# Kernel optimization log

Measured on AMD Instinct MI355X. Metric: run time of the kernel, lower is better.

Reference implementation:

```python
import jax, jax.numpy as jnp
import numpy as np

EMB = 128  # embsize
WORD = 128  # word_size
ITERS = 2


def _agg(embeds, neibors):
    # embeds: [B, N, D], neibors: [B, N, K] indices into node axis N (per batch)
    # mean-pool gathered neighbor embeddings -> [B, N, D]
    gathered = jax.vmap(lambda e, idx: e[idx])(embeds, neibors)  # [B, N, K, D]
    return gathered.mean(axis=2)


def setup_inputs() -> dict:
    key = jax.random.key(0)
    ks = jax.random.split(key, 9)
    B, N, K = 64, 512, 16
    word_embs = jax.random.normal(ks[0], (B, N, WORD), dtype=jnp.float32)
    lib_embs = jax.random.normal(ks[1], (B, N, WORD), dtype=jnp.float32)
    neibors = jax.random.randint(ks[2], (B, N, K), 0, N)
    neibors_lib = jax.random.randint(ks[3], (B, N, K), 0, N)
    mask = jax.random.uniform(ks[4], (B, N), dtype=jnp.float32)
    # xavier-uniform style params
    def xav(k, shape):
        bound = float(np.sqrt(6.0 / (shape[0] + shape[1])))
        return jax.random.uniform(k, shape, dtype=jnp.float32, minval=-bound, maxval=bound)
    weight = xav(ks[5], (WORD, EMB))
    weight2 = xav(ks[6], (EMB, EMB))
    enc_w1 = xav(ks[7], (WORD, EMB))
    enc_w2 = xav(ks[8], (EMB, EMB))
    return {"word_embs": word_embs, "neibors": neibors, "lib_embs": lib_embs,
            "neibors_lib": neibors_lib, "mask": mask, "weight": weight,
            "weight2": weight2, "enc_w1": enc_w1, "enc_w2": enc_w2}


def reference(word_embs, neibors, lib_embs, neibors_lib, mask, weight, weight2, enc_w1, enc_w2):
    B, N, _ = word_embs.shape
    # lib aggregation is loop-invariant (lib_embs fixed); same math as in-loop recompute
    agg_lib = jnp.einsum('bnw,we->bne', _agg(lib_embs, neibors_lib), weight)  # [B, N, EMB]
    word_proj = jnp.einsum('bnw,we->bne', word_embs, enc_w1)  # loop-invariant
    last_embed = jnp.zeros((B, N, EMB), dtype=jnp.float32)
    for _ in range(ITERS):
        agg_func = _agg(last_embed, neibors)  # [B, N, EMB]
        last_embed = jnp.tanh(word_proj + jnp.einsum('bne,ef->bnf', agg_func, enc_w2) + agg_lib)
    # masked sum over nodes, then final linear
    pooled = (last_embed * mask[:, :, None]).sum(axis=1)  # [B, EMB]
    return pooled @ weight2
```

## Files before the change

### kernel.cpp

```cpp
#include <hip/hip_runtime.h>
#include <hip/hip_bf16.h>

#define B_   64
#define N_   512
#define K_   16
#define D_   128
#define NPB  16
#define G1   ((B_*N_)/NPB)

typedef float f32x4  __attribute__((ext_vector_type(4)));
typedef short bf16x8 __attribute__((ext_vector_type(8)));

static __device__ __forceinline__ short f2bf(float x) {
    union { float f; unsigned u; } v; v.f = x;
    unsigned r = v.u + 0x7fffu + ((v.u >> 16) & 1u);
    return (short)(r >> 16);
}
static __device__ __forceinline__ float bfbits2f(unsigned hi_bits) {
    return __uint_as_float(hi_bits);
}
static __device__ __forceinline__ float fast_tanh(float x) {
    float e = __expf(2.f * x);
    return 1.f - 2.f * __builtin_amdgcn_rcpf(e + 1.f);
}

__global__ __launch_bounds__(256) void pack_kernel(const float* __restrict__ enc1,
                                                   const float* __restrict__ wgt,
                                                   const float* __restrict__ enc2,
                                                   short* __restrict__ Bp1,
                                                   short* __restrict__ Bp2,
                                                   float* __restrict__ out) {
    int tid = blockIdx.x * 256 + threadIdx.x;
    if (tid < 8192) out[tid] = 0.f;
    short o8[8];
    if (tid < 4096) {
        int l = tid & 63, nt = (tid >> 6) & 7, ks = tid >> 9;
        int k0 = ks * 32 + (l >> 4) * 8;
        int col = nt * 16 + (l & 15);
#pragma unroll
        for (int j = 0; j < 8; ++j) {
            int r = k0 + j;
            float v = (r < 128) ? enc1[r * 128 + col] : wgt[(r - 128) * 128 + col];
            o8[j] = f2bf(v);
        }
        *(int4*)&Bp1[(size_t)tid * 8] = *(int4*)o8;
    } else if (tid < 6144) {
        int t2 = tid - 4096;
        int l = t2 & 63, nt = (t2 >> 6) & 7, ks = t2 >> 9;
        int k0 = ks * 32 + (l >> 4) * 8;
        int col = nt * 16 + (l & 15);
#pragma unroll
        for (int j = 0; j < 8; ++j) o8[j] = f2bf(enc2[(k0 + j) * 128 + col]);
        *(int4*)&Bp2[(size_t)t2 * 8] = *(int4*)o8;
    }
}

static __device__ __forceinline__ int swz_blk() {
    const int hw = blockIdx.x;
    return ((hw & 7) << 8) + (hw >> 3);
}

#define LDA1 264
__global__ __launch_bounds__(256) void gemm1(const float* __restrict__ word,
                                             const int* __restrict__ nbrL,
                                             const float* __restrict__ lib,
                                             const short* __restrict__ Bp1,
                                             float* __restrict__ base,
                                             short* __restrict__ t1) {
    __shared__ short sA[NPB * LDA1];
    __shared__ int sIdx[NPB * 16];
    const int tid = threadIdx.x;
    const int blk = swz_blk();
    const int b = blk >> 5;
    const int node0 = blk * NPB;

    if (tid < 64) *(int4*)&sIdx[tid * 4] = *(const int4*)&nbrL[(size_t)node0 * 16 + tid * 4];
    __syncthreads();

    const int w = tid >> 6, l = tid & 63;
    const int rh = l >> 5, c4 = l & 31;
    const float* libB = lib + (size_t)b * N_ * D_;

#pragma unroll
    for (int p = 0; p < 2; ++p) {
        const int row = 4 * w + 2 * p + rh;
        const int gid = node0 + row;
        float4 wv = *(const float4*)&word[(size_t)gid * D_ + c4 * 4];
        short4 ws; ws.x = f2bf(wv.x); ws.y = f2bf(wv.y); ws.z = f2bf(wv.z); ws.w = f2bf(wv.w);
        *(short4*)&sA[row * LDA1 + c4 * 4] = ws;
        int idxr[16];
#pragma unroll
        for (int k = 0; k < 16; ++k) idxr[k] = sIdx[row * 16 + k];
        float4 s = {0.f, 0.f, 0.f, 0.f};
#pragma unroll
        for (int k = 0; k < 16; ++k) {
            float4 lv = *(const float4*)&libB[(size_t)idxr[k] * D_ + c4 * 4];
            s.x += lv.x; s.y += lv.y; s.z += lv.z; s.w += lv.w;
        }
        short4 as; as.x = f2bf(s.x * 0.0625f); as.y = f2bf(s.y * 0.0625f);
        as.z = f2bf(s.z * 0.0625f); as.w = f2bf(s.w * 0.0625f);
        *(short4*)&sA[row * LDA1 + 128 + c4 * 4] = as;
    }
    __syncthreads();

    f32x4 acc[2];
    acc[0] = (f32x4)0.f; acc[1] = (f32x4)0.f;

    const int arow = l & 15;
#pragma unroll
    for (int ks = 0; ks < 8; ++ks) {
        bf16x8 a = *(const bf16x8*)&sA[arow * LDA1 + ks * 32 + (l >> 4) * 8];
#pragma unroll
        for (int j = 0; j < 2; ++j) {
            const int nt = 2 * w + j;
            bf16x8 bb = *(const bf16x8*)&Bp1[((size_t)(ks * 8 + nt) * 64 + l) * 8];
            acc[j] = __builtin_amdgcn_mfma_f32_16x16x32_bf16(a, bb, acc[j], 0, 0, 0);
        }
    }

    const int r0 = (l >> 4) * 4;
    const int cl = l & 15;
#pragma unroll
    for (int j = 0; j < 2; ++j) {
        const int col = (2 * w + j) * 16 + cl;
#pragma unroll
        for (int r = 0; r < 4; ++r) {
            size_t o = (size_t)(node0 + r0 + r) * D_ + col;
            float v = acc[j][r];
            base[o] = v;
            t1[o] = f2bf(fast_tanh(v));
        }
    }
}

#define LDA2 136
__global__ __launch_bounds__(256) void gemm2(const short* __restrict__ t1,
                                             const int* __restrict__ nbr,
                                             const short* __restrict__ Bp2,
                                             const float* __restrict__ base,
                                             const float* __restrict__ mask,
                                             const float* __restrict__ w2,
                                             float* __restrict__ out) {
    __shared__ short sA[NPB * LDA2];
    __shared__ int sIdx[NPB * 16];
    __shared__ float pred[128];
    const int tid = threadIdx.x;
    const int blk = swz_blk();
    const int b = blk >> 5;
    const int node0 = blk * NPB;

    if (tid < 64) *(int4*)&sIdx[tid * 4] = *(const int4*)&nbr[(size_t)node0 * 16 + tid * 4];
    __syncthreads();

    const int w = tid >> 6, l = tid & 63;
    const int rh = l >> 5, c4 = l & 31;
    const short* t1B = t1 + (size_t)b * N_ * D_;

#pragma unroll
    for (int p = 0; p < 2; ++p) {
        const int row = 4 * w + 2 * p + rh;
        int idxr[16];
#pragma unroll
        for (int k = 0; k < 16; ++k) idxr[k] = sIdx[row * 16 + k];
        float s0 = 0.f, s1 = 0.f, s2 = 0.f, s3 = 0.f;
#pragma unroll
        for (int k = 0; k < 16; ++k) {
            uint2 u = *(const uint2*)&t1B[(size_t)idxr[k] * D_ + c4 * 4];
            s0 += bfbits2f(u.x << 16); s1 += bfbits2f(u.x & 0xffff0000u);
            s2 += bfbits2f(u.y << 16); s3 += bfbits2f(u.y & 0xffff0000u);
        }
        short4 as; as.x = f2bf(s0 * 0.0625f); as.y = f2bf(s1 * 0.0625f);
        as.z = f2bf(s2 * 0.0625f); as.w = f2bf(s3 * 0.0625f);
        *(short4*)&sA[row * LDA2 + c4 * 4] = as;
    }
    __syncthreads();

    f32x4 acc[2];
    acc[0] = (f32x4)0.f; acc[1] = (f32x4)0.f;

    const int arow = l & 15;
#pragma unroll
    for (int ks = 0; ks < 4; ++ks) {
        bf16x8 a = *(const bf16x8*)&sA[arow * LDA2 + ks * 32 + (l >> 4) * 8];
#pragma unroll
        for (int j = 0; j < 2; ++j) {
            const int nt = 2 * w + j;
            bf16x8 bb = *(const bf16x8*)&Bp2[((size_t)(ks * 8 + nt) * 64 + l) * 8];
            acc[j] = __builtin_amdgcn_mfma_f32_16x16x32_bf16(a, bb, acc[j], 0, 0, 0);
        }
    }

    const int r0 = (l >> 4) * 4;
    const int cl = l & 15;
#pragma unroll
    for (int j = 0; j < 2; ++j) {
        const int col = (2 * w + j) * 16 + cl;
        float s = 0.f;
#pragma unroll
        for (int r = 0; r < 4; ++r) {
            size_t o = (size_t)(node0 + r0 + r) * D_ + col;
            float v = fast_tanh(base[o] + acc[j][r]);
            s += v * mask[node0 + r0 + r];
        }
        s += __shfl_xor(s, 16);
        s += __shfl_xor(s, 32);
        if (l < 16) pred[col] = s;
    }
    __syncthreads();
    if (tid < 128) {
        float a2 = 0.f;
#pragma unroll 4
        for (int f = 0; f < 128; ++f) a2 += pred[f] * w2[f * 128 + tid];
        atomicAdd(&out[b * 128 + tid], a2);
    }
}

extern "C" void kernel_launch(void* const* d_in, const int* in_sizes, int n_in,
                              void* d_out, int out_size, void* d_ws, size_t ws_size,
                              hipStream_t stream) {
    const float* word_embs   = (const float*)d_in[0];
    const int*   neibors     = (const int*)d_in[1];
    const float* lib_embs    = (const float*)d_in[2];
    const int*   neibors_lib = (const int*)d_in[3];
    const float* mask        = (const float*)d_in[4];
    const float* weight      = (const float*)d_in[5];
    const float* weight2     = (const float*)d_in[6];
    const float* enc_w1      = (const float*)d_in[7];
    const float* enc_w2      = (const float*)d_in[8];
    float* out = (float*)d_out;

    char* ws = (char*)d_ws;
    float* base = (float*)(ws);
    short* t1   = (short*)(ws + (1u << 24));
    short* Bp1  = (short*)(ws + (1u << 24) + (1u << 23));
    short* Bp2  = (short*)(ws + (1u << 24) + (1u << 23) + 65536);

    pack_kernel<<<32, 256, 0, stream>>>(enc_w1, weight, enc_w2, Bp1, Bp2, out);
    gemm1<<<G1, 256, 0, stream>>>(word_embs, neibors_lib, lib_embs, Bp1, base, t1);
    gemm2<<<G1, 256, 0, stream>>>(t1, neibors, Bp2, base, mask, weight2, out);
}
```

Measured before the change: 51.28 us.

## Pre-convert lib embeddings to bf16 and store base intermediate in bf16

Adds a conversion pass in the prep kernel that turns lib_embs into a bf16 copy, so gemm1's neighbor gather reads half the bytes per neighbor. The base pre-activation written by gemm1 and reread by gemm2 is stored as bf16 instead of fp32, halving that round trip. The mask values are staged in shared memory. It adds an extra full pass over lib_embs and reduces the precision of the intermediate sums.

```diff
diff --git a/kernel.cpp b/kernel.cpp
--- a/kernel.cpp
+++ b/kernel.cpp
@@ -19,19 +19,38 @@
 static __device__ __forceinline__ float bfbits2f(unsigned hi_bits) {
     return __uint_as_float(hi_bits);
 }
+static __device__ __forceinline__ float bf2f(short h) {
+    return __uint_as_float(((unsigned)(unsigned short)h) << 16);
+}
 static __device__ __forceinline__ float fast_tanh(float x) {
     float e = __expf(2.f * x);
     return 1.f - 2.f * __builtin_amdgcn_rcpf(e + 1.f);
 }
 
-__global__ __launch_bounds__(256) void pack_kernel(const float* __restrict__ enc1,
-                                                   const float* __restrict__ wgt,
-                                                   const float* __restrict__ enc2,
-                                                   short* __restrict__ Bp1,
-                                                   short* __restrict__ Bp2,
-                                                   float* __restrict__ out) {
-    int tid = blockIdx.x * 256 + threadIdx.x;
-    if (tid < 8192) out[tid] = 0.f;
+__global__ __launch_bounds__(256) void prep(const float* __restrict__ lib,
+                                            const float* __restrict__ enc1,
+                                            const float* __restrict__ wgt,
+                                            const float* __restrict__ enc2,
+                                            short* __restrict__ libh,
+                                            short* __restrict__ Bp1,
+                                            short* __restrict__ Bp2,
+                                            float* __restrict__ out) {
+    const int blk = blockIdx.x;
+    if (blk < 1024) {
+        const size_t g = ((size_t)blk * 256 + threadIdx.x) * 16;
+        short o16[16];
+#pragma unroll
+        for (int q = 0; q < 4; ++q) {
+            float4 v = *(const float4*)&lib[g + q * 4];
+            o16[q * 4 + 0] = f2bf(v.x); o16[q * 4 + 1] = f2bf(v.y);
+            o16[q * 4 + 2] = f2bf(v.z); o16[q * 4 + 3] = f2bf(v.w);
+        }
+        *(int4*)&libh[g]     = *(int4*)o16;
+        *(int4*)&libh[g + 8] = *(int4*)(o16 + 8);
+        return;
+    }
+    int tid = (blk - 1024) * 256 + threadIdx.x;
+    out[tid] = 0.f;
     short o8[8];
     if (tid < 4096) {
         int l = tid & 63, nt = (tid >> 6) & 7, ks = tid >> 9;
@@ -63,9 +82,9 @@
 #define LDA1 264
 __global__ __launch_bounds__(256) void gemm1(const float* __restrict__ word,
                                              const int* __restrict__ nbrL,
-                                             const float* __restrict__ lib,
+                                             const short* __restrict__ libh,
                                              const short* __restrict__ Bp1,
-                                             float* __restrict__ base,
+                                             short* __restrict__ baseh,
                                              short* __restrict__ t1) {
     __shared__ short sA[NPB * LDA1];
     __shared__ int sIdx[NPB * 16];
@@ -79,7 +98,7 @@
 
     const int w = tid >> 6, l = tid & 63;
     const int rh = l >> 5, c4 = l & 31;
-    const float* libB = lib + (size_t)b * N_ * D_;
+    const short* libB = libh + (size_t)b * N_ * D_;
 
 #pragma unroll
     for (int p = 0; p < 2; ++p) {
@@ -91,14 +110,15 @@
         int idxr[16];
 #pragma unroll
         for (int k = 0; k < 16; ++k) idxr[k] = sIdx[row * 16 + k];
-        float4 s = {0.f, 0.f, 0.f, 0.f};
+        float s0 = 0.f, s1 = 0.f, s2 = 0.f, s3 = 0.f;
 #pragma unroll
         for (int k = 0; k < 16; ++k) {
-            float4 lv = *(const float4*)&libB[(size_t)idxr[k] * D_ + c4 * 4];
-            s.x += lv.x; s.y += lv.y; s.z += lv.z; s.w += lv.w;
-        }
-        short4 as; as.x = f2bf(s.x * 0.0625f); as.y = f2bf(s.y * 0.0625f);
-        as.z = f2bf(s.z * 0.0625f); as.w = f2bf(s.w * 0.0625f);
+            uint2 u = *(const uint2*)&libB[(size_t)idxr[k] * D_ + c4 * 4];
+            s0 += bfbits2f(u.x << 16); s1 += bfbits2f(u.x & 0xffff0000u);
+            s2 += bfbits2f(u.y << 16); s3 += bfbits2f(u.y & 0xffff0000u);
+        }
+        short4 as; as.x = f2bf(s0 * 0.0625f); as.y = f2bf(s1 * 0.0625f);
+        as.z = f2bf(s2 * 0.0625f); as.w = f2bf(s3 * 0.0625f);
         *(short4*)&sA[row * LDA1 + 128 + c4 * 4] = as;
     }
     __syncthreads();
@@ -127,8 +147,8 @@
         for (int r = 0; r < 4; ++r) {
             size_t o = (size_t)(node0 + r0 + r) * D_ + col;
             float v = acc[j][r];
-            base[o] = v;
-            t1[o] = f2bf(fast_tanh(v));
+            baseh[o] = f2bf(v);
+            t1[o]    = f2bf(fast_tanh(v));
         }
     }
 }
@@ -137,19 +157,21 @@
 __global__ __launch_bounds__(256) void gemm2(const short* __restrict__ t1,
                                              const int* __restrict__ nbr,
                                              const short* __restrict__ Bp2,
-                                             const float* __restrict__ base,
+                                             const short* __restrict__ baseh,
                                              const float* __restrict__ mask,
                                              const float* __restrict__ w2,
                                              float* __restrict__ out) {
     __shared__ short sA[NPB * LDA2];
     __shared__ int sIdx[NPB * 16];
     __shared__ float pred[128];
+    __shared__ float smask[NPB];
     const int tid = threadIdx.x;
     const int blk = swz_blk();
     const int b = blk >> 5;
     const int node0 = blk * NPB;
 
     if (tid < 64) *(int4*)&sIdx[tid * 4] = *(const int4*)&nbr[(size_t)node0 * 16 + tid * 4];
+    if (tid >= 64 && tid < 64 + NPB) smask[tid - 64] = mask[node0 + tid - 64];
     __syncthreads();
 
     const int w = tid >> 6, l = tid & 63;
@@ -199,8 +221,8 @@
 #pragma unroll
         for (int r = 0; r < 4; ++r) {
             size_t o = (size_t)(node0 + r0 + r) * D_ + col;
-            float v = fast_tanh(base[o] + acc[j][r]);
-            s += v * mask[node0 + r0 + r];
+            float v = fast_tanh(bf2f(baseh[o]) + acc[j][r]);
+            s += v * smask[r0 + r];
         }
         s += __shfl_xor(s, 16);
         s += __shfl_xor(s, 32);
@@ -230,12 +252,13 @@
     float* out = (float*)d_out;
 
     char* ws = (char*)d_ws;
-    float* base = (float*)(ws);
-    short* t1   = (short*)(ws + (1u << 24));
-    short* Bp1  = (short*)(ws + (1u << 24) + (1u << 23));
-    short* Bp2  = (short*)(ws + (1u << 24) + (1u << 23) + 65536);
-
-    pack_kernel<<<32, 256, 0, stream>>>(enc_w1, weight, enc_w2, Bp1, Bp2, out);
-    gemm1<<<G1, 256, 0, stream>>>(word_embs, neibors_lib, lib_embs, Bp1, base, t1);
-    gemm2<<<G1, 256, 0, stream>>>(t1, neibors, Bp2, base, mask, weight2, out);
-}
+    short* baseh = (short*)(ws);
+    short* t1    = (short*)(ws + (1u << 23));
+    short* libh  = (short*)(ws + (2u << 23));
+    short* Bp1   = (short*)(ws + (3u << 23));
+    short* Bp2   = (short*)(ws + (3u << 23) + 65536);
+
+    prep<<<1056, 256, 0, stream>>>(lib_embs, enc_w1, weight, enc_w2, libh, Bp1, Bp2, out);
+    gemm1<<<G1, 256, 0, stream>>>(word_embs, neibors_lib, libh, Bp1, baseh, t1);
+    gemm2<<<G1, 256, 0, stream>>>(t1, neibors, Bp2, baseh, mask, weight2, out);
+}
```

Result: faster. 49.59 us (-3.3%).

## Project before gathering so neighbor means run on projected bf16 rows

Applied to the files above, without the earlier changes.

Uses linearity of the mean to apply the weight projection before aggregation. A new proj kernel computes bf16 word_proj and lib_proj, k1 gathers the projected lib rows and multiplies tanh(base) by enc_w2, and k2 gathers those products and applies tanh, the mask and the final linear. This halves gather bytes (bf16 instead of fp32 lib rows) and removes the GEMM from the last stage. The cost is an extra kernel launch, an extra full pass writing and reading the projections, and more bf16 rounding in the base and product buffers.

```diff
diff --git a/kernel.cpp b/kernel.cpp
--- a/kernel.cpp
+++ b/kernel.cpp
@@ -5,8 +5,6 @@
 #define N_   512
 #define K_   16
 #define D_   128
-#define NPB  16
-#define G1   ((B_*N_)/NPB)
 
 typedef float f32x4  __attribute__((ext_vector_type(4)));
 typedef short bf16x8 __attribute__((ext_vector_type(8)));
@@ -19,39 +17,87 @@
 static __device__ __forceinline__ float bfbits2f(unsigned hi_bits) {
     return __uint_as_float(hi_bits);
 }
+static __device__ __forceinline__ float bf2f(short h) {
+    return __uint_as_float(((unsigned)(unsigned short)h) << 16);
+}
 static __device__ __forceinline__ float fast_tanh(float x) {
     float e = __expf(2.f * x);
     return 1.f - 2.f * __builtin_amdgcn_rcpf(e + 1.f);
 }
 
-__global__ __launch_bounds__(256) void pack_kernel(const float* __restrict__ enc1,
-                                                   const float* __restrict__ wgt,
-                                                   const float* __restrict__ enc2,
-                                                   short* __restrict__ Bp1,
-                                                   short* __restrict__ Bp2,
-                                                   float* __restrict__ out) {
-    int tid = blockIdx.x * 256 + threadIdx.x;
-    if (tid < 8192) out[tid] = 0.f;
+#define LDX 136
+
+__global__ __launch_bounds__(256) void pack(const float* __restrict__ enc1,
+                                            const float* __restrict__ wgt,
+                                            const float* __restrict__ enc2,
+                                            short* __restrict__ Bp1e,
+                                            short* __restrict__ Bpw,
+                                            short* __restrict__ Bp2,
+                                            float* __restrict__ out) {
+    const int blk = blockIdx.x, t = threadIdx.x;
+    if (blk >= 24) { out[(blk - 24) * 256 + t] = 0.f; return; }
+    const int ptid = blk * 256 + t;
+    const int m3 = ptid >> 11;
+    const int r = ptid & 2047;
+    const int ks = r >> 9, nt = (r >> 6) & 7, l = r & 63;
+    const int k0 = ks * 32 + (l >> 4) * 8;
+    const int col = nt * 16 + (l & 15);
+    const float* src = (m3 == 0) ? enc1 : (m3 == 1) ? wgt : enc2;
+    short* dst = (m3 == 0) ? Bp1e : (m3 == 1) ? Bpw : Bp2;
     short o8[8];
-    if (tid < 4096) {
-        int l = tid & 63, nt = (tid >> 6) & 7, ks = tid >> 9;
-        int k0 = ks * 32 + (l >> 4) * 8;
-        int col = nt * 16 + (l & 15);
-#pragma unroll
-        for (int j = 0; j < 8; ++j) {
-            int r = k0 + j;
-            float v = (r < 128) ? enc1[r * 128 + col] : wgt[(r - 128) * 128 + col];
-            o8[j] = f2bf(v);
-        }
-        *(int4*)&Bp1[(size_t)tid * 8] = *(int4*)o8;
-    } else if (tid < 6144) {
-        int t2 = tid - 4096;
-        int l = t2 & 63, nt = (t2 >> 6) & 7, ks = t2 >> 9;
-        int k0 = ks * 32 + (l >> 4) * 8;
-        int col = nt * 16 + (l & 15);
-#pragma unroll
-        for (int j = 0; j < 8; ++j) o8[j] = f2bf(enc2[(k0 + j) * 128 + col]);
-        *(int4*)&Bp2[(size_t)t2 * 8] = *(int4*)o8;
+#pragma unroll
+    for (int j = 0; j < 8; ++j) o8[j] = f2bf(src[(k0 + j) * 128 + col]);
+    *(int4*)&dst[(size_t)r * 8] = *(int4*)o8;
+}
+
+__global__ __launch_bounds__(256) void proj(const float* __restrict__ word,
+                                            const float* __restrict__ lib,
+                                            const short* __restrict__ Bp1e,
+                                            const short* __restrict__ Bpw,
+                                            short* __restrict__ wordp,
+                                            short* __restrict__ libp) {
+    __shared__ short sX[16 * LDX];
+    const int hw = blockIdx.x, t = threadIdx.x;
+    const int g = hw & 7, q = hw >> 3;
+    const int m = q >> 8;
+    const int Lb = g * 256 + (q & 255);
+    const float* X = m ? lib : word;
+    const short* Bp = m ? Bpw : Bp1e;
+    short* Y = m ? libp : wordp;
+    const size_t rb = (size_t)Lb * 16;
+
+#pragma unroll
+    for (int i = 0; i < 2; ++i) {
+        const int gidx = i * 1024 + t * 4;
+        const int row = gidx >> 7, col = gidx & 127;
+        float4 v = *(const float4*)&X[rb * 128 + gidx];
+        short4 s; s.x = f2bf(v.x); s.y = f2bf(v.y); s.z = f2bf(v.z); s.w = f2bf(v.w);
+        *(short4*)&sX[row * LDX + col] = s;
+    }
+    __syncthreads();
+
+    const int w = t >> 6, l = t & 63;
+    f32x4 acc[2];
+    acc[0] = (f32x4)0.f; acc[1] = (f32x4)0.f;
+    const int arow = l & 15;
+#pragma unroll
+    for (int ks = 0; ks < 4; ++ks) {
+        bf16x8 a = *(const bf16x8*)&sX[arow * LDX + ks * 32 + (l >> 4) * 8];
+#pragma unroll
+        for (int j = 0; j < 2; ++j) {
+            const int nt = 2 * w + j;
+            bf16x8 bb = *(const bf16x8*)&Bp[((size_t)(ks * 8 + nt) * 64 + l) * 8];
+            acc[j] = __builtin_amdgcn_mfma_f32_16x16x32_bf16(a, bb, acc[j], 0, 0, 0);
+        }
+    }
+
+    const int r0 = (l >> 4) * 4, cl = l & 15;
+#pragma unroll
+    for (int j = 0; j < 2; ++j) {
+        const int col = (2 * w + j) * 16 + cl;
+#pragma unroll
+        for (int r = 0; r < 4; ++r)
+            Y[(rb + r0 + r) * 128 + col] = f2bf(acc[j][r]);
     }
 }
 
@@ -60,102 +106,100 @@
     return ((hw & 7) << 8) + (hw >> 3);
 }
 
-#define LDA1 264
-__global__ __launch_bounds__(256) void gemm1(const float* __restrict__ word,
-                                             const int* __restrict__ nbrL,
-                                             const float* __restrict__ lib,
-                                             const short* __restrict__ Bp1,
-                                             float* __restrict__ base,
-                                             short* __restrict__ t1) {
-    __shared__ short sA[NPB * LDA1];
-    __shared__ int sIdx[NPB * 16];
+__global__ __launch_bounds__(256) void k1(const int* __restrict__ nbrL,
+                                          const short* __restrict__ libp,
+                                          const short* __restrict__ wordp,
+                                          const short* __restrict__ Bp2,
+                                          short* __restrict__ baseh,
+                                          short* __restrict__ u) {
+    __shared__ short sA[16 * LDX];
+    __shared__ int sIdx[16 * 16];
     const int tid = threadIdx.x;
     const int blk = swz_blk();
     const int b = blk >> 5;
-    const int node0 = blk * NPB;
+    const int node0 = blk * 16;
 
     if (tid < 64) *(int4*)&sIdx[tid * 4] = *(const int4*)&nbrL[(size_t)node0 * 16 + tid * 4];
     __syncthreads();
 
     const int w = tid >> 6, l = tid & 63;
     const int rh = l >> 5, c4 = l & 31;
-    const float* libB = lib + (size_t)b * N_ * D_;
+    const short* libB = libp + (size_t)b * N_ * D_;
 
 #pragma unroll
     for (int p = 0; p < 2; ++p) {
         const int row = 4 * w + 2 * p + rh;
-        const int gid = node0 + row;
-        float4 wv = *(const float4*)&word[(size_t)gid * D_ + c4 * 4];
-        short4 ws; ws.x = f2bf(wv.x); ws.y = f2bf(wv.y); ws.z = f2bf(wv.z); ws.w = f2bf(wv.w);
-        *(short4*)&sA[row * LDA1 + c4 * 4] = ws;
         int idxr[16];
 #pragma unroll
         for (int k = 0; k < 16; ++k) idxr[k] = sIdx[row * 16 + k];
-        float4 s = {0.f, 0.f, 0.f, 0.f};
+        float s0 = 0.f, s1 = 0.f, s2 = 0.f, s3 = 0.f;
 #pragma unroll
         for (int k = 0; k < 16; ++k) {
-            float4 lv = *(const float4*)&libB[(size_t)idxr[k] * D_ + c4 * 4];
-            s.x += lv.x; s.y += lv.y; s.z += lv.z; s.w += lv.w;
-        }
-        short4 as; as.x = f2bf(s.x * 0.0625f); as.y = f2bf(s.y * 0.0625f);
-        as.z = f2bf(s.z * 0.0625f); as.w = f2bf(s.w * 0.0625f);
-        *(short4*)&sA[row * LDA1 + 128 + c4 * 4] = as;
+            uint2 uu = *(const uint2*)&libB[(size_t)idxr[k] * D_ + c4 * 4];
+            s0 += bfbits2f(uu.x << 16); s1 += bfbits2f(uu.x & 0xffff0000u);
+            s2 += bfbits2f(uu.y << 16); s3 += bfbits2f(uu.y & 0xffff0000u);
+        }
+        short4 wp = *(const short4*)&wordp[(size_t)(node0 + row) * D_ + c4 * 4];
+        float b0 = bf2f(wp.x) + s0 * 0.0625f;
+        float b1 = bf2f(wp.y) + s1 * 0.0625f;
+        float b2 = bf2f(wp.z) + s2 * 0.0625f;
+        float b3 = bf2f(wp.w) + s3 * 0.0625f;
+        short4 bs; bs.x = f2bf(b0); bs.y = f2bf(b1); bs.z = f2bf(b2); bs.w = f2bf(b3);
+        *(short4*)&baseh[(size_t)(node0 + row) * D_ + c4 * 4] = bs;
+        short4 ts; ts.x = f2bf(fast_tanh(b0)); ts.y = f2bf(fast_tanh(b1));
+        ts.z = f2bf(fast_tanh(b2)); ts.w = f2bf(fast_tanh(b3));
+        *(short4*)&sA[row * LDX + c4 * 4] = ts;
     }
     __syncthreads();
 
     f32x4 acc[2];
     acc[0] = (f32x4)0.f; acc[1] = (f32x4)0.f;
-
     const int arow = l & 15;
 #pragma unroll
-    for (int ks = 0; ks < 8; ++ks) {
-        bf16x8 a = *(const bf16x8*)&sA[arow * LDA1 + ks * 32 + (l >> 4) * 8];
+    for (int ks = 0; ks < 4; ++ks) {
+        bf16x8 a = *(const bf16x8*)&sA[arow * LDX + ks * 32 + (l >> 4) * 8];
 #pragma unroll
         for (int j = 0; j < 2; ++j) {
             const int nt = 2 * w + j;
-            bf16x8 bb = *(const bf16x8*)&Bp1[((size_t)(ks * 8 + nt) * 64 + l) * 8];
+            bf16x8 bb = *(const bf16x8*)&Bp2[((size_t)(ks * 8 + nt) * 64 + l) * 8];
             acc[j] = __builtin_amdgcn_mfma_f32_16x16x32_bf16(a, bb, acc[j], 0, 0, 0);
         }
     }
 
-    const int r0 = (l >> 4) * 4;
-    const int cl = l & 15;
+    const int r0 = (l >> 4) * 4, cl = l & 15;
 #pragma unroll
     for (int j = 0; j < 2; ++j) {
         const int col = (2 * w + j) * 16 + cl;
 #pragma unroll
-        for (int r = 0; r < 4; ++r) {
-            size_t o = (size_t)(node0 + r0 + r) * D_ + col;
-            float v = acc[j][r];
-            base[o] = v;
-            t1[o] = f2bf(fast_tanh(v));
-        }
-    }
-}
-
-#define LDA2 136
-__global__ __launch_bounds__(256) void gemm2(const short* __restrict__ t1,
-                                             const int* __restrict__ nbr,
-                                             const short* __restrict__ Bp2,
-                                             const float* __restrict__ base,
-                                             const float* __restrict__ mask,
-                                             const float* __restrict__ w2,
-                                             float* __restrict__ out) {
-    __shared__ short sA[NPB * LDA2];
-    __shared__ int sIdx[NPB * 16];
+        for (int r = 0; r < 4; ++r)
+            u[(size_t)(node0 + r0 + r) * D_ + col] = f2bf(acc[j][r]);
+    }
+}
+
+__global__ __launch_bounds__(256) void k2(const int* __restrict__ nbr,
+                                          const short* __restrict__ u,
+                                          const short* __restrict__ baseh,
+                                          const float* __restrict__ mask,
+                                          const float* __restrict__ w2,
+                                          float* __restrict__ out) {
+    __shared__ int sIdx[16 * 16];
+    __shared__ float smask[16];
+    __shared__ float predp[8][128];
     __shared__ float pred[128];
     const int tid = threadIdx.x;
     const int blk = swz_blk();
     const int b = blk >> 5;
-    const int node0 = blk * NPB;
+    const int node0 = blk * 16;
 
     if (tid < 64) *(int4*)&sIdx[tid * 4] = *(const int4*)&nbr[(size_t)node0 * 16 + tid * 4];
+    if (tid >= 64 && tid < 80) smask[tid - 64] = mask[node0 + tid - 64];
     __syncthreads();
 
     const int w = tid >> 6, l = tid & 63;
     const int rh = l >> 5, c4 = l & 31;
-    const short* t1B = t1 + (size_t)b * N_ * D_;
-
+    const short* uB = u + (size_t)b * N_ * D_;
+
+    float a0 = 0.f, a1 = 0.f, a2c = 0.f, a3 = 0.f;
 #pragma unroll
     for (int p = 0; p < 2; ++p) {
         const int row = 4 * w + 2 * p + rh;
@@ -165,53 +209,36 @@
         float s0 = 0.f, s1 = 0.f, s2 = 0.f, s3 = 0.f;
 #pragma unroll
         for (int k = 0; k < 16; ++k) {
-            uint2 u = *(const uint2*)&t1B[(size_t)idxr[k] * D_ + c4 * 4];
-            s0 += bfbits2f(u.x << 16); s1 += bfbits2f(u.x & 0xffff0000u);
-            s2 += bfbits2f(u.y << 16); s3 += bfbits2f(u.y & 0xffff0000u);
-        }
-        short4 as; as.x = f2bf(s0 * 0.0625f); as.y = f2bf(s1 * 0.0625f);
-        as.z = f2bf(s2 * 0.0625f); as.w = f2bf(s3 * 0.0625f);
-        *(short4*)&sA[row * LDA2 + c4 * 4] = as;
-    }
-    __syncthreads();
-
-    f32x4 acc[2];
-    acc[0] = (f32x4)0.f; acc[1] = (f32x4)0.f;
-
-    const int arow = l & 15;
-#pragma unroll
-    for (int ks = 0; ks < 4; ++ks) {
-        bf16x8 a = *(const bf16x8*)&sA[arow * LDA2 + ks * 32 + (l >> 4) * 8];
-#pragma unroll
-        for (int j = 0; j < 2; ++j) {
-            const int nt = 2 * w + j;
-            bf16x8 bb = *(const bf16x8*)&Bp2[((size_t)(ks * 8 + nt) * 64 + l) * 8];
-            acc[j] = __builtin_amdgcn_mfma_f32_16x16x32_bf16(a, bb, acc[j], 0, 0, 0);
-        }
-    }
-
-    const int r0 = (l >> 4) * 4;
-    const int cl = l & 15;
-#pragma unroll
-    for (int j = 0; j < 2; ++j) {
-        const int col = (2 * w + j) * 16 + cl;
-        float s = 0.f;
-#pragma unroll
-        for (int r = 0; r < 4; ++r) {
-            size_t o = (size_t)(node0 + r0 + r) * D_ + col;
-            float v = fast_tanh(base[o] + acc[j][r]);
-            s += v * mask[node0 + r0 + r];
-        }
-        s += __shfl_xor(s, 16);
-        s += __shfl_xor(s, 32);
-        if (l < 16) pred[col] = s;
-    }
-    __syncthreads();
+            uint2 uu = *(const uint2*)&uB[(size_t)idxr[k] * D_ + c4 * 4];
+            s0 += bfbits2f(uu.x << 16); s1 += bfbits2f(uu.x & 0xffff0000u);
+            s2 += bfbits2f(uu.y << 16); s3 += bfbits2f(uu.y & 0xffff0000u);
+        }
+        short4 bs = *(const short4*)&baseh[(size_t)(node0 + row) * D_ + c4 * 4];
+        const float mk = smask[row];
+        a0 += mk * fast_tanh(bf2f(bs.x) + s0 * 0.0625f);
+        a1 += mk * fast_tanh(bf2f(bs.y) + s1 * 0.0625f);
+        a2c += mk * fast_tanh(bf2f(bs.z) + s2 * 0.0625f);
+        a3 += mk * fast_tanh(bf2f(bs.w) + s3 * 0.0625f);
+    }
+    const int pg = w * 2 + rh;
+    predp[pg][c4 * 4 + 0] = a0;
+    predp[pg][c4 * 4 + 1] = a1;
+    predp[pg][c4 * 4 + 2] = a2c;
+    predp[pg][c4 * 4 + 3] = a3;
+    __syncthreads();
+
     if (tid < 128) {
-        float a2 = 0.f;
+        float tot = 0.f;
+#pragma unroll
+        for (int pgi = 0; pgi < 8; ++pgi) tot += predp[pgi][tid];
+        pred[tid] = tot;
+    }
+    __syncthreads();
+    if (tid < 128) {
+        float acc = 0.f;
 #pragma unroll 4
-        for (int f = 0; f < 128; ++f) a2 += pred[f] * w2[f * 128 + tid];
-        atomicAdd(&out[b * 128 + tid], a2);
+        for (int f = 0; f < 128; ++f) acc += pred[f] * w2[f * 128 + tid];
+        atomicAdd(&out[b * 128 + tid], acc);
     }
 }
 
@@ -230,12 +257,16 @@
     float* out = (float*)d_out;
 
     char* ws = (char*)d_ws;
-    float* base = (float*)(ws);
-    short* t1   = (short*)(ws + (1u << 24));
-    short* Bp1  = (short*)(ws + (1u << 24) + (1u << 23));
-    short* Bp2  = (short*)(ws + (1u << 24) + (1u << 23) + 65536);
-
-    pack_kernel<<<32, 256, 0, stream>>>(enc_w1, weight, enc_w2, Bp1, Bp2, out);
-    gemm1<<<G1, 256, 0, stream>>>(word_embs, neibors_lib, lib_embs, Bp1, base, t1);
-    gemm2<<<G1, 256, 0, stream>>>(t1, neibors, Bp2, base, mask, weight2, out);
-}
+    short* wordp = (short*)(ws);
+    short* libp  = (short*)(ws + (1u << 23));
+    short* ubuf  = (short*)(ws + (2u << 23));
+    short* baseh = (short*)(ws + (3u << 23));
+    short* Bp1e  = (short*)(ws + (4u << 23));
+    short* Bpw   = (short*)(ws + (4u << 23) + 32768);
+    short* Bp2   = (short*)(ws + (4u << 23) + 65536);
+
+    pack<<<56, 256, 0, stream>>>(enc_w1, weight, enc_w2, Bp1e, Bpw, Bp2, out);
+    proj<<<4096, 256, 0, stream>>>(word_embs, lib_embs, Bp1e, Bpw, wordp, libp);
+    k1<<<2048, 256, 0, stream>>>(neibors_lib, libp, wordp, Bp2, baseh, ubuf);
+    k2<<<2048, 256, 0, stream>>>(neibors, ubuf, baseh, mask, weight2, out);
+}
```

Result: slower. 56.01 us (+9.2%).

## Swap intermediate precisions: store base as bf16 and tanh output as fp32

Applied to the files above, without the earlier changes.

The intermediate buffers change precision. The pre-activation base is now stored as bf16, while the first-iteration tanh output t1 is stored as fp32 so the gather in gemm2 reads float4 values instead of unpacking bf16. The gather-sum loops use packed v_pk_add_f32 through inline asm and load neighbor indices as int4. Mask values are staged in shared memory, and the pack kernel gets a dedicated range of blocks to zero the output. Total bytes written stay about the same, but gemm2's random gather now moves twice as many bytes while its streaming read of base halves.

```diff
diff --git a/kernel.cpp b/kernel.cpp
--- a/kernel.cpp
+++ b/kernel.cpp
@@ -16,22 +16,27 @@
     unsigned r = v.u + 0x7fffu + ((v.u >> 16) & 1u);
     return (short)(r >> 16);
 }
-static __device__ __forceinline__ float bfbits2f(unsigned hi_bits) {
-    return __uint_as_float(hi_bits);
+static __device__ __forceinline__ float bf2f(short h) {
+    return __uint_as_float(((unsigned)(unsigned short)h) << 16);
 }
 static __device__ __forceinline__ float fast_tanh(float x) {
     float e = __expf(2.f * x);
     return 1.f - 2.f * __builtin_amdgcn_rcpf(e + 1.f);
 }
-
-__global__ __launch_bounds__(256) void pack_kernel(const float* __restrict__ enc1,
-                                                   const float* __restrict__ wgt,
-                                                   const float* __restrict__ enc2,
-                                                   short* __restrict__ Bp1,
-                                                   short* __restrict__ Bp2,
-                                                   float* __restrict__ out) {
-    int tid = blockIdx.x * 256 + threadIdx.x;
-    if (tid < 8192) out[tid] = 0.f;
+static __device__ __forceinline__ void pk_add(float2& acc, float x, float y) {
+    float2 v; v.x = x; v.y = y;
+    asm("v_pk_add_f32 %0, %1, %0" : "+v"(acc) : "v"(v));
+}
+
+__global__ __launch_bounds__(256) void pack(const float* __restrict__ enc1,
+                                            const float* __restrict__ wgt,
+                                            const float* __restrict__ enc2,
+                                            short* __restrict__ Bp1,
+                                            short* __restrict__ Bp2,
+                                            float* __restrict__ out) {
+    const int blk = blockIdx.x, t = threadIdx.x;
+    if (blk >= 24) { out[(blk - 24) * 256 + t] = 0.f; return; }
+    int tid = blk * 256 + t;
     short o8[8];
     if (tid < 4096) {
         int l = tid & 63, nt = (tid >> 6) & 7, ks = tid >> 9;
@@ -44,7 +49,7 @@
             o8[j] = f2bf(v);
         }
         *(int4*)&Bp1[(size_t)tid * 8] = *(int4*)o8;
-    } else if (tid < 6144) {
+    } else {
         int t2 = tid - 4096;
         int l = t2 & 63, nt = (t2 >> 6) & 7, ks = t2 >> 9;
         int k0 = ks * 32 + (l >> 4) * 8;
@@ -61,12 +66,14 @@
 }
 
 #define LDA1 264
+#define LDA2 136
+
 __global__ __launch_bounds__(256) void gemm1(const float* __restrict__ word,
                                              const int* __restrict__ nbrL,
                                              const float* __restrict__ lib,
                                              const short* __restrict__ Bp1,
-                                             float* __restrict__ base,
-                                             short* __restrict__ t1) {
+                                             short* __restrict__ baseh,
+                                             float* __restrict__ t1f) {
     __shared__ short sA[NPB * LDA1];
     __shared__ int sIdx[NPB * 16];
     const int tid = threadIdx.x;
@@ -90,22 +97,22 @@
         *(short4*)&sA[row * LDA1 + c4 * 4] = ws;
         int idxr[16];
 #pragma unroll
-        for (int k = 0; k < 16; ++k) idxr[k] = sIdx[row * 16 + k];
-        float4 s = {0.f, 0.f, 0.f, 0.f};
+        for (int q = 0; q < 4; ++q) *(int4*)&idxr[q * 4] = *(const int4*)&sIdx[row * 16 + q * 4];
+        float2 a01 = {0.f, 0.f}, a23 = {0.f, 0.f};
 #pragma unroll
         for (int k = 0; k < 16; ++k) {
             float4 lv = *(const float4*)&libB[(size_t)idxr[k] * D_ + c4 * 4];
-            s.x += lv.x; s.y += lv.y; s.z += lv.z; s.w += lv.w;
-        }
-        short4 as; as.x = f2bf(s.x * 0.0625f); as.y = f2bf(s.y * 0.0625f);
-        as.z = f2bf(s.z * 0.0625f); as.w = f2bf(s.w * 0.0625f);
+            pk_add(a01, lv.x, lv.y);
+            pk_add(a23, lv.z, lv.w);
+        }
+        short4 as; as.x = f2bf(a01.x * 0.0625f); as.y = f2bf(a01.y * 0.0625f);
+        as.z = f2bf(a23.x * 0.0625f); as.w = f2bf(a23.y * 0.0625f);
         *(short4*)&sA[row * LDA1 + 128 + c4 * 4] = as;
     }
     __syncthreads();
 
     f32x4 acc[2];
     acc[0] = (f32x4)0.f; acc[1] = (f32x4)0.f;
-
     const int arow = l & 15;
 #pragma unroll
     for (int ks = 0; ks < 8; ++ks) {
@@ -127,57 +134,57 @@
         for (int r = 0; r < 4; ++r) {
             size_t o = (size_t)(node0 + r0 + r) * D_ + col;
             float v = acc[j][r];
-            base[o] = v;
-            t1[o] = f2bf(fast_tanh(v));
-        }
-    }
-}
-
-#define LDA2 136
-__global__ __launch_bounds__(256) void gemm2(const short* __restrict__ t1,
+            baseh[o] = f2bf(v);
+            t1f[o]   = fast_tanh(v);
+        }
+    }
+}
+
+__global__ __launch_bounds__(256) void gemm2(const float* __restrict__ t1f,
                                              const int* __restrict__ nbr,
                                              const short* __restrict__ Bp2,
-                                             const float* __restrict__ base,
+                                             const short* __restrict__ baseh,
                                              const float* __restrict__ mask,
                                              const float* __restrict__ w2,
                                              float* __restrict__ out) {
     __shared__ short sA[NPB * LDA2];
     __shared__ int sIdx[NPB * 16];
     __shared__ float pred[128];
+    __shared__ float smask[NPB];
     const int tid = threadIdx.x;
     const int blk = swz_blk();
     const int b = blk >> 5;
     const int node0 = blk * NPB;
 
     if (tid < 64) *(int4*)&sIdx[tid * 4] = *(const int4*)&nbr[(size_t)node0 * 16 + tid * 4];
+    if (tid >= 64 && tid < 64 + NPB) smask[tid - 64] = mask[node0 + tid - 64];
     __syncthreads();
 
     const int w = tid >> 6, l = tid & 63;
     const int rh = l >> 5, c4 = l & 31;
-    const short* t1B = t1 + (size_t)b * N_ * D_;
+    const float* t1B = t1f + (size_t)b * N_ * D_;
 
 #pragma unroll
     for (int p = 0; p < 2; ++p) {
         const int row = 4 * w + 2 * p + rh;
         int idxr[16];
 #pragma unroll
-        for (int k = 0; k < 16; ++k) idxr[k] = sIdx[row * 16 + k];
-        float s0 = 0.f, s1 = 0.f, s2 = 0.f, s3 = 0.f;
+        for (int q = 0; q < 4; ++q) *(int4*)&idxr[q * 4] = *(const int4*)&sIdx[row * 16 + q * 4];
+        float2 a01 = {0.f, 0.f}, a23 = {0.f, 0.f};
 #pragma unroll
         for (int k = 0; k < 16; ++k) {
-            uint2 u = *(const uint2*)&t1B[(size_t)idxr[k] * D_ + c4 * 4];
-            s0 += bfbits2f(u.x << 16); s1 += bfbits2f(u.x & 0xffff0000u);
-            s2 += bfbits2f(u.y << 16); s3 += bfbits2f(u.y & 0xffff0000u);
-        }
-        short4 as; as.x = f2bf(s0 * 0.0625f); as.y = f2bf(s1 * 0.0625f);
-        as.z = f2bf(s2 * 0.0625f); as.w = f2bf(s3 * 0.0625f);
+            float4 lv = *(const float4*)&t1B[(size_t)idxr[k] * D_ + c4 * 4];
+            pk_add(a01, lv.x, lv.y);
+            pk_add(a23, lv.z, lv.w);
+        }
+        short4 as; as.x = f2bf(a01.x * 0.0625f); as.y = f2bf(a01.y * 0.0625f);
+        as.z = f2bf(a23.x * 0.0625f); as.w = f2bf(a23.y * 0.0625f);
         *(short4*)&sA[row * LDA2 + c4 * 4] = as;
     }
     __syncthreads();
 
     f32x4 acc[2];
     acc[0] = (f32x4)0.f; acc[1] = (f32x4)0.f;
-
     const int arow = l & 15;
 #pragma unroll
     for (int ks = 0; ks < 4; ++ks) {
@@ -199,8 +206,8 @@
 #pragma unroll
         for (int r = 0; r < 4; ++r) {
             size_t o = (size_t)(node0 + r0 + r) * D_ + col;
-            float v = fast_tanh(base[o] + acc[j][r]);
-            s += v * mask[node0 + r0 + r];
+            float v = fast_tanh(bf2f(baseh[o]) + acc[j][r]);
+            s += v * smask[r0 + r];
         }
         s += __shfl_xor(s, 16);
         s += __shfl_xor(s, 32);
@@ -230,12 +237,12 @@
     float* out = (float*)d_out;
 
     char* ws = (char*)d_ws;
-    float* base = (float*)(ws);
-    short* t1   = (short*)(ws + (1u << 24));
-    short* Bp1  = (short*)(ws + (1u << 24) + (1u << 23));
-    short* Bp2  = (short*)(ws + (1u << 24) + (1u << 23) + 65536);
-
-    pack_kernel<<<32, 256, 0, stream>>>(enc_w1, weight, enc_w2, Bp1, Bp2, out);
-    gemm1<<<G1, 256, 0, stream>>>(word_embs, neibors_lib, lib_embs, Bp1, base, t1);
-    gemm2<<<G1, 256, 0, stream>>>(t1, neibors, Bp2, base, mask, weight2, out);
-}
+    short* baseh = (short*)(ws);
+    float* t1f   = (float*)(ws + (1u << 23));
+    short* Bp1   = (short*)(ws + (3u << 23));
+    short* Bp2   = (short*)(ws + (3u << 23) + 65536);
+
+    pack<<<56, 256, 0, stream>>>(enc_w1, weight, enc_w2, Bp1, Bp2, out);
+    gemm1<<<G1, 256, 0, stream>>>(word_embs, neibors_lib, lib_embs, Bp1, baseh, t1f);
+    gemm2<<<G1, 256, 0, stream>>>(t1f, neibors, Bp2, baseh, mask, weight2, out);
+}
```

After: 53.47 us. +4.3%, slower.
